# Kernel optimization log

Measured on AMD Instinct MI355X. Metric: run time of the kernel, lower is better.

## Reference

```python
import jax, jax.numpy as jnp
import numpy as np

EPS = 1e-5
SLOPE = 0.2  # leaky_relu negative_slope


def _mesh_conv_face(fe, gemm, w, b):
    # fe: [B, C, F]; gemm: [B, F, 3] neighbor face indices; w: [O, C, 4]; b: [O]
    # Gather 3 neighbor faces per face (irregular access).
    nb = jax.vmap(lambda f, g: f[:, g])(fe, gemm)  # [B, C, F, 3]
    n1, n2, n3 = nb[..., 0], nb[..., 1], nb[..., 2]
    # Symmetric (order-invariant) feature columns over the 3 neighbors.
    G = jnp.stack(
        [
            fe,                                                        # center face
            n1 + n2 + n3,                                              # sum
            jnp.abs(n1 - n2) + jnp.abs(n2 - n3) + jnp.abs(n3 - n1),    # pairwise abs-diff sum
            jnp.maximum(n1, jnp.maximum(n2, n3)),                      # max
        ],
        axis=-1,
    )  # [B, C, F, 4]
    # Conv2d with kernel (1,4) == contraction over (C, 4).
    return jnp.einsum('bcfk,ock->bof', G, w) + b[None, :, None]  # [B, O, F]


def _bn(x, gamma, beta):
    # BatchNorm2d (training mode) on [B, C, F]; normalize per-channel over (B, F).
    mu = x.mean(axis=(0, 2), keepdims=True)
    var = x.var(axis=(0, 2), keepdims=True)  # biased, as torch uses for normalization
    xn = (x - mu) * jax.lax.rsqrt(var + EPS)
    return gamma[None, :, None] * xn + beta[None, :, None]


def _lrelu(x):
    return jnp.where(x >= 0, x, SLOPE * x)


def setup_inputs() -> dict:
    key = jax.random.key(0)
    ks = jax.random.split(key, 8)
    B, Cin, Cout, F = 4, 32, 64, 50000
    fe = jax.random.normal(ks[0], (B, Cin, F), dtype=jnp.float32)
    gemm = jax.random.randint(ks[1], (B, F, 3), 0, F)
    w1 = jax.random.normal(ks[2], (Cout, Cin, 4), dtype=jnp.float32) * 0.05
    w2a = jax.random.normal(ks[3], (Cout, Cout, 4), dtype=jnp.float32) * 0.05
    w2b = jax.random.normal(ks[4], (Cout, Cout, 4), dtype=jnp.float32) * 0.05
    z = jnp.zeros((Cout,), jnp.float32)
    o = jnp.ones((Cout,), jnp.float32)
    return {
        'fe': fe, 'gemm': gemm,
        'w1': w1, 'b1': z, 'w2a': w2a, 'b2a': z, 'w2b': w2b, 'b2b': z,
        'g0': o, 'be0': z, 'g1': o, 'be1': z, 'g2': o, 'be2': z,
    }


def reference(fe, gemm, w1, b1, w2a, b2a, w2b, b2b, g0, be0, g1, be1, g2, be2):
    # conv1 -> BN -> LeakyReLU
    x1 = _lrelu(_bn(_mesh_conv_face(fe, gemm, w1, b1), g0, be0))
    # residual block 1
    x2 = _lrelu(_bn(_mesh_conv_face(x1, gemm, w2a, b2a), g1, be1) + x1)
    x1 = x2
    # residual block 2
    x2 = _lrelu(_bn(_mesh_conv_face(x1, gemm, w2b, b2b), g2, be2) + x1)
    return x2  # [B, Cout, F]; pool=0 so before_pool is None
```

## Files before the change

kernel.cpp:

```cpp
#include <hip/hip_runtime.h>
#include <hip/hip_bf16.h>
#include <math.h>


typedef __attribute__((ext_vector_type(8))) short short8;
typedef __attribute__((ext_vector_type(8))) unsigned short ushort8_t;
typedef __attribute__((ext_vector_type(4))) float f32x4;

__device__ inline unsigned short f2bf(float v) {
    union { float f; unsigned u; } x; x.f = v;
    unsigned r = x.u + 0x7fffu + ((x.u >> 16) & 1u);
    return (unsigned short)(r >> 16);
}
__device__ inline float bf2f(unsigned short u) {
    union { unsigned u; float f; } x; x.u = ((unsigned)u) << 16; return x.f;
}
__device__ inline unsigned pk2(float a, float b) {
    union { __hip_bfloat162 h; unsigned u; } c;
    c.h = __float22bfloat162_rn(make_float2(a, b));
    return c.u;
}

__global__ void transpose_fe_kernel(const float* __restrict__ fe,
                                    unsigned short* __restrict__ o, int F,
                                    const float* __restrict__ w1,
                                    const float* __restrict__ w2a,
                                    const float* __restrict__ w2b,
                                    unsigned short* __restrict__ w1b,
                                    unsigned short* __restrict__ w2ab,
                                    unsigned short* __restrict__ w2bb)
{
    __shared__ float tile[64 * 33];
    const int b = blockIdx.y;
    const int f0 = blockIdx.x * 64;
    const int t = threadIdx.x;

    {
        const int bid = blockIdx.y * gridDim.x + blockIdx.x;
        if (bid < 32)       { const int i = bid * 256 + t;        w1b[i]  = f2bf(w1[i]);  }
        else if (bid < 96)  { const int i = (bid - 32) * 256 + t; w2ab[i] = f2bf(w2a[i]); }
        else if (bid < 160) { const int i = (bid - 96) * 256 + t; w2bb[i] = f2bf(w2b[i]); }
    }

    const int lane = t & 63;
    const int w = t >> 6;
    const int f = f0 + lane;
    if (f < F) {
#pragma unroll
        for (int i = 0; i < 8; ++i) {
            const int c = w * 8 + i;
            tile[lane * 33 + c] = fe[((size_t)b * 32 + c) * F + f];
        }
    }
    __syncthreads();
    const int j = t >> 2, s = t & 3;
    const int fj = f0 + j;
    if (fj < F) {
        unsigned fw[4];
#pragma unroll
        for (int i = 0; i < 4; ++i)
            fw[i] = pk2(tile[j * 33 + s * 8 + 2 * i], tile[j * 33 + s * 8 + 2 * i + 1]);
        *(uint4*)(o + ((size_t)b * F + fj) * 32 + s * 8) = make_uint4(fw[0], fw[1], fw[2], fw[3]);
    }
}

template <int CIN, bool NORM>
__launch_bounds__(256, (CIN == 32) ? 5 : (NORM ? 3 : 4))
__global__ void conv_mfma_kernel(const unsigned short* __restrict__ x,
                                 const int*   __restrict__ gidx,
                                 const unsigned short* __restrict__ wb,
                                 const float* __restrict__ bias,
                                 const float* __restrict__ mrIn,
                                 unsigned short* __restrict__ y,
                                 float* __restrict__ pS,
                                 float* __restrict__ pQ,
                                 int nb, int nbx, int F)
{
    constexpr int NSEG = CIN / 32;
    constexpr int K    = 4 * CIN;
    constexpr int RB   = 2 * K;
    constexpr int GB   = 64 * RB;
    constexpr int GREG = (GB > 17408) ? GB : 17408;
    __shared__ __align__(16) unsigned char smem[GREG];
    float* tile = (float*)smem;

    const int NBg = gridDim.x;
    const int t = threadIdx.x;
    const int j = t >> 2, s = t & 3;
    const int lane = t & 63, wv = t >> 6;
    const int l15 = lane & 15, quad = lane >> 4;
    const int kb = quad * 8;

    unsigned char* grow = smem + j * RB;
    const int swz = (j & 7) << 4;

    const int bpx  = NBg >> 3;
    const int xcd  = blockIdx.x & 7, slot = blockIdx.x >> 3;
    const int qq   = nb >> 3, rr = nb & 7;
    const int lo   = (xcd < rr) ? xcd * (qq + 1) : rr * (qq + 1) + (xcd - rr) * qq;
    const int L    = qq + (xcd < rr ? 1 : 0);

    short8 afr[K / 32];
    {
        const int ar = wv * 16 + l15;
#pragma unroll
        for (int ksi = 0; ksi < K / 32; ++ksi)
            afr[ksi] = *(const short8*)(wb + (size_t)ar * K + ksi * 32 + kb);
    }
    const f32x4 bias4 = *(const f32x4*)(bias + wv * 16 + quad * 4);

    float scr[NSEG * 8], shr[NSEG * 8];
    if constexpr (NORM) {
#pragma unroll
        for (int i = 0; i < NSEG; ++i) {
            const int c0 = (i * 4 + s) * 8;
#pragma unroll
            for (int h = 0; h < 2; ++h) {
                const f32x4 a  = *(const f32x4*)(mrIn + c0 + 4 * h);
                const f32x4 sh = *(const f32x4*)(mrIn + 64 + c0 + 4 * h);
#pragma unroll
                for (int q = 0; q < 4; ++q) {
                    scr[i * 8 + 4 * h + q] = a[q];
                    shr[i * 8 + 4 * h + q] = sh[q];
                }
            }
        }
    }

    ushort8_t vc[NSEG], v0[NSEG], v1[NSEG], v2[NSEG];
    int gA0, gA1, gA2;
    float S_acc = 0.f, Q_acc = 0.f;
    const int so = t & 63, sg = t >> 6;

    int u = slot;

    if (u < L) {
        {
            const int tl = lo + u;
            const int b0 = tl / nbx;
            const int f0 = (tl - b0 * nbx) * 64;
            const int fc = min(f0 + j, F - 1);
            const int* gp = gidx + ((size_t)b0 * F + fc) * 3;
            const int g0 = gp[0], g1 = gp[1], g2 = gp[2];
            const unsigned short* xb = x + (size_t)b0 * F * CIN;
            const unsigned short* pc = xb + (size_t)fc * CIN;
            const unsigned short* p0 = xb + (size_t)g0 * CIN;
            const unsigned short* p1 = xb + (size_t)g1 * CIN;
            const unsigned short* p2 = xb + (size_t)g2 * CIN;
#pragma unroll
            for (int i = 0; i < NSEG; ++i) {
                const int c0 = (i * 4 + s) * 8;
                vc[i] = *(const ushort8_t*)(pc + c0);
                v0[i] = *(const ushort8_t*)(p0 + c0);
                v1[i] = *(const ushort8_t*)(p1 + c0);
                v2[i] = *(const ushort8_t*)(p2 + c0);
            }
        }
        {
            const int tn = lo + min(u + bpx, L - 1);
            const int bn = tn / nbx;
            const int fn = min((tn - bn * nbx) * 64 + j, F - 1);
            const int* gp = gidx + ((size_t)bn * F + fn) * 3;
            gA0 = gp[0]; gA1 = gp[1]; gA2 = gp[2];
        }
    }

    for (; u < L; u += bpx) {
        const int tl = lo + u;
        const int b  = tl / nbx;
        const int f0 = (tl - b * nbx) * 64;

#pragma unroll
        for (int i = 0; i < NSEG; ++i) {
            const int c0 = (i * 4 + s) * 8;
            unsigned fw[16];
#pragma unroll
            for (int q = 0; q < 8; ++q) {
                float ctr = bf2f(vc[i][q]);
                float a   = bf2f(v0[i][q]);
                float bb  = bf2f(v1[i][q]);
                float cc  = bf2f(v2[i][q]);
                if constexpr (NORM) {
                    const float sc_ = scr[i * 8 + q], sh_ = shr[i * 8 + q];
                    ctr = fmaf(ctr, sc_, sh_); ctr = fmaxf(ctr, 0.2f * ctr);
                    a   = fmaf(a,   sc_, sh_); a   = fmaxf(a,   0.2f * a);
                    bb  = fmaf(bb,  sc_, sh_); bb  = fmaxf(bb,  0.2f * bb);
                    cc  = fmaf(cc,  sc_, sh_); cc  = fmaxf(cc,  0.2f * cc);
                }
                const float su = a + bb + cc;
                const float dd = fabsf(a - bb) + fabsf(bb - cc) + fabsf(cc - a);
                const float mm = fmaxf(a, fmaxf(bb, cc));
                fw[2 * q]     = pk2(ctr, su);
                fw[2 * q + 1] = pk2(dd, mm);
            }
#pragma unroll
            for (int q4 = 0; q4 < 4; ++q4) {
                const int qb = 8 * c0 + 16 * q4;
                *(uint4*)(grow + (qb ^ swz)) =
                    make_uint4(fw[4 * q4], fw[4 * q4 + 1], fw[4 * q4 + 2], fw[4 * q4 + 3]);
            }
        }

        {
            const int tn = lo + min(u + bpx, L - 1);
            const int bn = tn / nbx;
            const int fcn = min((tn - bn * nbx) * 64 + j, F - 1);
            const unsigned short* xb = x + (size_t)bn * F * CIN;
            const unsigned short* pc = xb + (size_t)fcn * CIN;
            const unsigned short* p0 = xb + (size_t)gA0 * CIN;
            const unsigned short* p1 = xb + (size_t)gA1 * CIN;
            const unsigned short* p2 = xb + (size_t)gA2 * CIN;
#pragma unroll
            for (int i = 0; i < NSEG; ++i) {
                const int c0 = (i * 4 + s) * 8;
                vc[i] = *(const ushort8_t*)(pc + c0);
                v0[i] = *(const ushort8_t*)(p0 + c0);
                v1[i] = *(const ushort8_t*)(p1 + c0);
                v2[i] = *(const ushort8_t*)(p2 + c0);
            }
            const int t2 = lo + min(u + 2 * bpx, L - 1);
            const int b2 = t2 / nbx;
            const int f2 = min((t2 - b2 * nbx) * 64 + j, F - 1);
            const int* gp = gidx + ((size_t)b2 * F + f2) * 3;
            gA0 = gp[0]; gA1 = gp[1]; gA2 = gp[2];
        }
        __syncthreads();

        f32x4 acc[4];
#pragma unroll
        for (int nt = 0; nt < 4; ++nt) acc[nt] = (f32x4){0.f, 0.f, 0.f, 0.f};
#pragma unroll
        for (int ksi = 0; ksi < K / 32; ++ksi) {
            const int cb = 2 * (ksi * 32 + kb);
#pragma unroll
            for (int nt = 0; nt < 4; ++nt) {
                const int nr = nt * 16 + l15;
                const short8 bfr = *(const short8*)(smem + nr * RB + (cb ^ ((nr & 7) << 4)));
                acc[nt] = __builtin_amdgcn_mfma_f32_16x16x32_bf16(afr[ksi], bfr, acc[nt], 0, 0, 0);
            }
        }
        __syncthreads();

        {
            const int cb0 = wv * 16 + quad * 4;
#pragma unroll
            for (int nt = 0; nt < 4; ++nt) {
                const int face = nt * 16 + l15;
                *(f32x4*)(tile + face * 68 + cb0) = acc[nt] + bias4;
            }
        }
        __syncthreads();
        {
#pragma unroll
            for (int i = 0; i < 16; ++i) {
                const int f = sg + 4 * i;
                if (f0 + f < F) {
                    const float v = tile[f * 68 + so];
                    S_acc += v; Q_acc += v * v;
                }
            }
        }
        {
            const int f = f0 + j;
            if (f < F) {
                unsigned fw[8];
#pragma unroll
                for (int ii = 0; ii < 8; ++ii)
                    fw[ii] = pk2(tile[j * 68 + s * 16 + 2 * ii],
                                 tile[j * 68 + s * 16 + 2 * ii + 1]);
                unsigned short* yp = y + ((size_t)b * F + f) * 64 + s * 16;
                *(uint4*)yp       = make_uint4(fw[0], fw[1], fw[2], fw[3]);
                *(uint4*)(yp + 8) = make_uint4(fw[4], fw[5], fw[6], fw[7]);
            }
        }
        __syncthreads();
    }

    float* redS = (float*)smem;
    float* redQ = redS + 256;
    redS[t] = S_acc; redQ[t] = Q_acc;
    __syncthreads();
    if (t < 64) {
        pS[(size_t)blockIdx.x * 64 + t] = redS[t] + redS[64 + t] + redS[128 + t] + redS[192 + t];
        pQ[(size_t)blockIdx.x * 64 + t] = redQ[t] + redQ[64 + t] + redQ[128 + t] + redQ[192 + t];
    }
}

__global__ void finalize_kernel(const float* __restrict__ pS, const float* __restrict__ pQ,
                                int nbg, float invN,
                                const float* __restrict__ gamma,
                                const float* __restrict__ beta,
                                float* __restrict__ mr)
{
    __shared__ float rs_[256], rq_[256];
    const int o = blockIdx.x, t = threadIdx.x;
    float S = 0.f, Q = 0.f;
    for (int jj = t; jj < nbg; jj += 256) {
        S += pS[(size_t)jj * 64 + o];
        Q += pQ[(size_t)jj * 64 + o];
    }
    rs_[t] = S; rq_[t] = Q;
    __syncthreads();
#pragma unroll
    for (int s = 128; s > 0; s >>= 1) {
        if (t < s) { rs_[t] += rs_[t + s]; rq_[t] += rq_[t + s]; }
        __syncthreads();
    }
    if (t == 0) {
        const float mu  = rs_[0] * invN;
        const float var = rq_[0] * invN - mu * mu;
        const float rsg = rsqrtf(var + 1e-5f);
        const float sc  = gamma[o] * rsg;
        mr[o]      = sc;
        mr[64 + o] = fmaf(-sc, mu, beta[o]);
    }
}

__global__ void norm_res_kernel(const unsigned short* __restrict__ y1,
                                const unsigned short* __restrict__ y2,
                                const float* __restrict__ mr1,
                                const float* __restrict__ mr2,
                                unsigned short* __restrict__ out,
                                int N8)
{
    const int tid = blockIdx.x * blockDim.x + threadIdx.x;
    if (tid >= N8) return;
    const int c0 = (tid & 7) * 8;
    const ushort8_t a = *(const ushort8_t*)(y1 + (size_t)tid * 8);
    const ushort8_t b = *(const ushort8_t*)(y2 + (size_t)tid * 8);
    float r[8];
#pragma unroll
    for (int h = 0; h < 2; ++h) {
        const f32x4 s1 = *(const f32x4*)(mr1 + c0 + 4 * h);
        const f32x4 h1 = *(const f32x4*)(mr1 + 64 + c0 + 4 * h);
        const f32x4 s2 = *(const f32x4*)(mr2 + c0 + 4 * h);
        const f32x4 h2 = *(const f32x4*)(mr2 + 64 + c0 + 4 * h);
#pragma unroll
        for (int i = 0; i < 4; ++i) {
            float x1 = fmaf(bf2f(a[4 * h + i]), s1[i], h1[i]);
            x1 = fmaxf(x1, 0.2f * x1);
            float v = fmaf(bf2f(b[4 * h + i]), s2[i], h2[i]) + x1;
            r[4 * h + i] = fmaxf(v, 0.2f * v);
        }
    }
    unsigned fw[4];
#pragma unroll
    for (int i = 0; i < 4; ++i) fw[i] = pk2(r[2 * i], r[2 * i + 1]);
    *(uint4*)(out + (size_t)tid * 8) = make_uint4(fw[0], fw[1], fw[2], fw[3]);
}

__global__ void norm_transpose_kernel(const unsigned short* __restrict__ y,
                                      const unsigned short* __restrict__ res,
                                      const float* __restrict__ mr,
                                      float* __restrict__ out, int F)
{
    __shared__ float tile[64 * 65];
    const int b = blockIdx.y, f0 = blockIdx.x * 64, t = threadIdx.x;
    const int j = t >> 2, s = t & 3;
    const int f = f0 + j;
    if (f < F) {
        const size_t row = ((size_t)b * F + f) * 64;
#pragma unroll
        for (int i = 0; i < 2; ++i) {
            const int c0 = s * 16 + i * 8;
            const ushort8_t yv = *(const ushort8_t*)(y + row + c0);
            const ushort8_t rv = *(const ushort8_t*)(res + row + c0);
#pragma unroll
            for (int h = 0; h < 2; ++h) {
                const f32x4 sc = *(const f32x4*)(mr + c0 + 4 * h);
                const f32x4 sh = *(const f32x4*)(mr + 64 + c0 + 4 * h);
#pragma unroll
                for (int q = 0; q < 4; ++q) {
                    float vv = fmaf(bf2f(yv[4 * h + q]), sc[q], sh[q]) + bf2f(rv[4 * h + q]);
                    vv = fmaxf(vv, 0.2f * vv);
                    tile[(c0 + 4 * h + q) * 65 + j] = vv;
                }
            }
        }
    }
    __syncthreads();
    const int o = t >> 2;
    float* ob = out + ((size_t)b * 64 + o) * F + f0;
#pragma unroll
    for (int i = 0; i < 4; ++i) {
        const int fs = (i * 4 + s) * 4;
        if (f0 + fs < F) {
            f32x4 v;
#pragma unroll
            for (int q = 0; q < 4; ++q) v[q] = tile[o * 65 + fs + q];
            *(f32x4*)(ob + fs) = v;
        }
    }
}

extern "C" void kernel_launch(void* const* d_in, const int* in_sizes, int n_in,
                              void* d_out, int out_size, void* d_ws, size_t ws_size,
                              hipStream_t stream)
{
    const float* fe  = (const float*)d_in[0];
    const int*   gm  = (const int*)d_in[1];
    const float* w1  = (const float*)d_in[2];
    const float* b1  = (const float*)d_in[3];
    const float* w2a = (const float*)d_in[4];
    const float* b2a = (const float*)d_in[5];
    const float* w2b = (const float*)d_in[6];
    const float* b2b = (const float*)d_in[7];
    const float* g0  = (const float*)d_in[8];
    const float* be0 = (const float*)d_in[9];
    const float* g1  = (const float*)d_in[10];
    const float* be1 = (const float*)d_in[11];
    const float* g2  = (const float*)d_in[12];
    const float* be2 = (const float*)d_in[13];

    const int B = 4, O = 64;
    const int F = in_sizes[0] / (B * 32);
    const int M = B * F;
    const float invN = 1.0f / (float)M;
    const int nbx = (F + 63) / 64;
    const int nb  = nbx * B;

    unsigned short* Y1 = (unsigned short*)d_ws;
    unsigned short* Y2 = Y1 + (size_t)M * O;
    unsigned short* x2 = Y2 + (size_t)M * O;
    float* pS  = (float*)(x2 + (size_t)M * O);
    float* pQ  = pS + 2048 * 64;
    float* mr1 = pQ + 2048 * 64;
    float* mr2 = mr1 + 128;
    float* mr3 = mr2 + 128;
    unsigned short* w1b  = (unsigned short*)(mr3 + 128);
    unsigned short* w2ab = w1b + 64 * 128;
    unsigned short* w2bb = w2ab + 64 * 256;
    unsigned short* fe_t = (unsigned short*)d_out;

    dim3 blk(256);
    dim3 tgrid(nbx, B);
    const int N8 = M * 8;
    dim3 ngrid((N8 + 255) / 256);
    const int g1g = (nb < 1280) ? (nb & ~7) : 1280;
    const int g2g = (nb < 768)  ? (nb & ~7) : 768;
    const int g3g = (nb < 1024) ? (nb & ~7) : 1024;

    transpose_fe_kernel<<<tgrid, blk, 0, stream>>>(fe, fe_t, F,
                                                   w1, w2a, w2b, w1b, w2ab, w2bb);

    conv_mfma_kernel<32, false><<<g1g, blk, 0, stream>>>(
        fe_t, gm, w1b, b1, nullptr, Y1, pS, pQ, nb, nbx, F);
    finalize_kernel<<<64, 256, 0, stream>>>(pS, pQ, g1g, invN, g0, be0, mr1);

    conv_mfma_kernel<64, true><<<g2g, blk, 0, stream>>>(
        Y1, gm, w2ab, b2a, mr1, Y2, pS, pQ, nb, nbx, F);
    finalize_kernel<<<64, 256, 0, stream>>>(pS, pQ, g2g, invN, g1, be1, mr2);

    norm_res_kernel<<<ngrid, blk, 0, stream>>>(Y1, Y2, mr1, mr2, x2, N8);

    conv_mfma_kernel<64, false><<<g3g, blk, 0, stream>>>(
        x2, gm, w2bb, b2b, nullptr, Y1, pS, pQ, nb, nbx, F);
    finalize_kernel<<<64, 256, 0, stream>>>(pS, pQ, g3g, invN, g2, be2, mr3);

    norm_transpose_kernel<<<tgrid, blk, 0, stream>>>(Y1, x2, mr3, (float*)d_out, F);
}
```

Measured before the change: 216.3 us.

## Double-buffer neighbor gathers with ping-pong register sets in conv loop

Replaces the single register set for gathered center/neighbor features with two alternating sets (A/B). The gather for the next tile is issued before the current tile's feature build and MFMA, not after it. The loop is manually unrolled by two via macros. The aim is to hide more irregular gather latency behind compute. The cost is doubled gather registers, which may lower occupancy or cause spills, especially for CIN=64.

Result: slower. 232.8 us (+7.6%).

```diff
diff --git a/kernel.cpp b/kernel.cpp
--- a/kernel.cpp
+++ b/kernel.cpp
@@ -63,6 +63,119 @@
         *(uint4*)(o + ((size_t)b * F + fj) * 32 + s * 8) = make_uint4(fw[0], fw[1], fw[2], fw[3]);
     }
 }
+
+#define LOAD_IDX(gg0, gg1, gg2, TT) do {                                   \
+    const int tn_ = lo + min((TT), L - 1);                                 \
+    const int bn_ = tn_ / nbx;                                             \
+    const int fn_ = min((tn_ - bn_ * nbx) * 64 + j, F - 1);                \
+    const int* gp_ = gidx + ((size_t)bn_ * F + fn_) * 3;                   \
+    gg0 = gp_[0]; gg1 = gp_[1]; gg2 = gp_[2];                              \
+} while (0)
+
+#define ISSUE_G(SET, gg0, gg1, gg2, TT) do {                               \
+    const int tn_ = lo + min((TT), L - 1);                                 \
+    const int bn_ = tn_ / nbx;                                             \
+    const int fcn_ = min((tn_ - bn_ * nbx) * 64 + j, F - 1);               \
+    const unsigned short* xb_ = x + (size_t)bn_ * F * CIN;                 \
+    const unsigned short* pc_ = xb_ + (size_t)fcn_ * CIN;                  \
+    const unsigned short* p0_ = xb_ + (size_t)(gg0) * CIN;                 \
+    const unsigned short* p1_ = xb_ + (size_t)(gg1) * CIN;                 \
+    const unsigned short* p2_ = xb_ + (size_t)(gg2) * CIN;                 \
+    _Pragma("unroll")                                                      \
+    for (int i_ = 0; i_ < NSEG; ++i_) {                                    \
+        const int c0_ = (i_ * 4 + s) * 8;                                  \
+        SET##c[i_]  = *(const ushort8_t*)(pc_ + c0_);                      \
+        SET##n0[i_] = *(const ushort8_t*)(p0_ + c0_);                      \
+        SET##n1[i_] = *(const ushort8_t*)(p1_ + c0_);                      \
+        SET##n2[i_] = *(const ushort8_t*)(p2_ + c0_);                      \
+    }                                                                      \
+} while (0)
+
+#define TILE_BODY(SET, go0, go1, go2, gn0, gn1, gn2, UU) do {              \
+    const int tl_ = lo + (UU);                                             \
+    const int b_  = tl_ / nbx;                                             \
+    const int f0_ = (tl_ - b_ * nbx) * 64;                                 \
+    LOAD_IDX(gn0, gn1, gn2, (UU) + 2 * bpx);                               \
+    _Pragma("unroll")                                                      \
+    for (int i_ = 0; i_ < NSEG; ++i_) {                                    \
+        const int c0_ = (i_ * 4 + s) * 8;                                  \
+        unsigned fw_[16];                                                  \
+        _Pragma("unroll")                                                  \
+        for (int q_ = 0; q_ < 8; ++q_) {                                   \
+            float ctr_ = bf2f(SET##c[i_][q_]);                             \
+            float a_   = bf2f(SET##n0[i_][q_]);                            \
+            float bb_  = bf2f(SET##n1[i_][q_]);                            \
+            float cc_  = bf2f(SET##n2[i_][q_]);                            \
+            if constexpr (NORM) {                                          \
+                const float sc_ = scr[i_ * 8 + q_], sh_ = shr[i_ * 8 + q_];\
+                ctr_ = fmaf(ctr_, sc_, sh_); ctr_ = fmaxf(ctr_, 0.2f * ctr_);\
+                a_   = fmaf(a_,   sc_, sh_); a_   = fmaxf(a_,   0.2f * a_);\
+                bb_  = fmaf(bb_,  sc_, sh_); bb_  = fmaxf(bb_,  0.2f * bb_);\
+                cc_  = fmaf(cc_,  sc_, sh_); cc_  = fmaxf(cc_,  0.2f * cc_);\
+            }                                                              \
+            const float su_ = a_ + bb_ + cc_;                              \
+            const float dd_ = fabsf(a_ - bb_) + fabsf(bb_ - cc_) + fabsf(cc_ - a_);\
+            const float mm_ = fmaxf(a_, fmaxf(bb_, cc_));                  \
+            fw_[2 * q_]     = pk2(ctr_, su_);                              \
+            fw_[2 * q_ + 1] = pk2(dd_, mm_);                               \
+        }                                                                  \
+        _Pragma("unroll")                                                  \
+        for (int q4_ = 0; q4_ < 4; ++q4_) {                                \
+            const int qb_ = 8 * c0_ + 16 * q4_;                            \
+            *(uint4*)(grow + (qb_ ^ swz)) =                                \
+                make_uint4(fw_[4 * q4_], fw_[4 * q4_ + 1],                 \
+                           fw_[4 * q4_ + 2], fw_[4 * q4_ + 3]);            \
+        }                                                                  \
+    }                                                                      \
+    __syncthreads();                                      \
+    f32x4 acc_[4];                                                         \
+    _Pragma("unroll")                                                      \
+    for (int nt_ = 0; nt_ < 4; ++nt_) acc_[nt_] = (f32x4){0.f,0.f,0.f,0.f};\
+    _Pragma("unroll")                                                      \
+    for (int ksi_ = 0; ksi_ < K / 32; ++ksi_) {                            \
+        const int cb_ = 2 * (ksi_ * 32 + kb);                              \
+        _Pragma("unroll")                                                  \
+        for (int nt_ = 0; nt_ < 4; ++nt_) {                                \
+            const int nr_ = nt_ * 16 + l15;                                \
+            const short8 bfr_ = *(const short8*)(smem + nr_ * RB + (cb_ ^ ((nr_ & 7) << 4)));\
+            acc_[nt_] = __builtin_amdgcn_mfma_f32_16x16x32_bf16(afr[ksi_], bfr_, acc_[nt_], 0, 0, 0);\
+        }                                                                  \
+    }                                                                      \
+    __syncthreads();                                    \
+    {                                                                      \
+        const int cb0_ = wv * 16 + quad * 4;                               \
+        _Pragma("unroll")                                                  \
+        for (int nt_ = 0; nt_ < 4; ++nt_) {                                \
+            const int face_ = nt_ * 16 + l15;                              \
+            *(f32x4*)(tile + face_ * 68 + cb0_) = acc_[nt_] + bias4;       \
+        }                                                                  \
+    }                                                                      \
+    __syncthreads();                                   \
+    {                                                                      \
+        _Pragma("unroll")                                                  \
+        for (int i_ = 0; i_ < 16; ++i_) {                                  \
+            const int f_ = sg + 4 * i_;                                    \
+            if (f0_ + f_ < F) {                                            \
+                const float v_ = tile[f_ * 68 + so];                       \
+                S_acc += v_; Q_acc += v_ * v_;                             \
+            }                                                              \
+        }                                                                  \
+    }                                                                      \
+    {                                                                      \
+        const int f_ = f0_ + j;                                            \
+        if (f_ < F) {                                                      \
+            unsigned fw_[8];                                               \
+            _Pragma("unroll")                                              \
+            for (int ii_ = 0; ii_ < 8; ++ii_)                              \
+                fw_[ii_] = pk2(tile[j * 68 + s * 16 + 2 * ii_],            \
+                               tile[j * 68 + s * 16 + 2 * ii_ + 1]);       \
+            unsigned short* yp_ = y + ((size_t)b_ * F + f_) * 64 + s * 16; \
+            *(uint4*)yp_       = make_uint4(fw_[0], fw_[1], fw_[2], fw_[3]);\
+            *(uint4*)(yp_ + 8) = make_uint4(fw_[4], fw_[5], fw_[6], fw_[7]);\
+        }                                                                  \
+    }                                                                      \
+    __syncthreads();                                    \
+} while (0)
 
 template <int CIN, bool NORM>
 __launch_bounds__(256, (CIN == 32) ? 5 : (NORM ? 3 : 4))
@@ -127,155 +240,30 @@
         }
     }
 
-    ushort8_t vc[NSEG], v0[NSEG], v1[NSEG], v2[NSEG];
-    int gA0, gA1, gA2;
+    ushort8_t Ac[NSEG], An0[NSEG], An1[NSEG], An2[NSEG];
+    ushort8_t Bc[NSEG], Bn0[NSEG], Bn1[NSEG], Bn2[NSEG];
+    int gA0, gA1, gA2, gB0, gB1, gB2;
     float S_acc = 0.f, Q_acc = 0.f;
     const int so = t & 63, sg = t >> 6;
 
     int u = slot;
-
     if (u < L) {
-        {
-            const int tl = lo + u;
-            const int b0 = tl / nbx;
-            const int f0 = (tl - b0 * nbx) * 64;
-            const int fc = min(f0 + j, F - 1);
-            const int* gp = gidx + ((size_t)b0 * F + fc) * 3;
-            const int g0 = gp[0], g1 = gp[1], g2 = gp[2];
-            const unsigned short* xb = x + (size_t)b0 * F * CIN;
-            const unsigned short* pc = xb + (size_t)fc * CIN;
-            const unsigned short* p0 = xb + (size_t)g0 * CIN;
-            const unsigned short* p1 = xb + (size_t)g1 * CIN;
-            const unsigned short* p2 = xb + (size_t)g2 * CIN;
-#pragma unroll
-            for (int i = 0; i < NSEG; ++i) {
-                const int c0 = (i * 4 + s) * 8;
-                vc[i] = *(const ushort8_t*)(pc + c0);
-                v0[i] = *(const ushort8_t*)(p0 + c0);
-                v1[i] = *(const ushort8_t*)(p1 + c0);
-                v2[i] = *(const ushort8_t*)(p2 + c0);
-            }
-        }
-        {
-            const int tn = lo + min(u + bpx, L - 1);
-            const int bn = tn / nbx;
-            const int fn = min((tn - bn * nbx) * 64 + j, F - 1);
-            const int* gp = gidx + ((size_t)bn * F + fn) * 3;
-            gA0 = gp[0]; gA1 = gp[1]; gA2 = gp[2];
-        }
-    }
-
-    for (; u < L; u += bpx) {
-        const int tl = lo + u;
-        const int b  = tl / nbx;
-        const int f0 = (tl - b * nbx) * 64;
-
-#pragma unroll
-        for (int i = 0; i < NSEG; ++i) {
-            const int c0 = (i * 4 + s) * 8;
-            unsigned fw[16];
-#pragma unroll
-            for (int q = 0; q < 8; ++q) {
-                float ctr = bf2f(vc[i][q]);
-                float a   = bf2f(v0[i][q]);
-                float bb  = bf2f(v1[i][q]);
-                float cc  = bf2f(v2[i][q]);
-                if constexpr (NORM) {
-                    const float sc_ = scr[i * 8 + q], sh_ = shr[i * 8 + q];
-                    ctr = fmaf(ctr, sc_, sh_); ctr = fmaxf(ctr, 0.2f * ctr);
-                    a   = fmaf(a,   sc_, sh_); a   = fmaxf(a,   0.2f * a);
-                    bb  = fmaf(bb,  sc_, sh_); bb  = fmaxf(bb,  0.2f * bb);
-                    cc  = fmaf(cc,  sc_, sh_); cc  = fmaxf(cc,  0.2f * cc);
-                }
-                const float su = a + bb + cc;
-                const float dd = fabsf(a - bb) + fabsf(bb - cc) + fabsf(cc - a);
-                const float mm = fmaxf(a, fmaxf(bb, cc));
-                fw[2 * q]     = pk2(ctr, su);
-                fw[2 * q + 1] = pk2(dd, mm);
-            }
-#pragma unroll
-            for (int q4 = 0; q4 < 4; ++q4) {
-                const int qb = 8 * c0 + 16 * q4;
-                *(uint4*)(grow + (qb ^ swz)) =
-                    make_uint4(fw[4 * q4], fw[4 * q4 + 1], fw[4 * q4 + 2], fw[4 * q4 + 3]);
-            }
-        }
-
-        {
-            const int tn = lo + min(u + bpx, L - 1);
-            const int bn = tn / nbx;
-            const int fcn = min((tn - bn * nbx) * 64 + j, F - 1);
-            const unsigned short* xb = x + (size_t)bn * F * CIN;
-            const unsigned short* pc = xb + (size_t)fcn * CIN;
-            const unsigned short* p0 = xb + (size_t)gA0 * CIN;
-            const unsigned short* p1 = xb + (size_t)gA1 * CIN;
-            const unsigned short* p2 = xb + (size_t)gA2 * CIN;
-#pragma unroll
-            for (int i = 0; i < NSEG; ++i) {
-                const int c0 = (i * 4 + s) * 8;
-                vc[i] = *(const ushort8_t*)(pc + c0);
-                v0[i] = *(const ushort8_t*)(p0 + c0);
-                v1[i] = *(const ushort8_t*)(p1 + c0);
-                v2[i] = *(const ushort8_t*)(p2 + c0);
-            }
-            const int t2 = lo + min(u + 2 * bpx, L - 1);
-            const int b2 = t2 / nbx;
-            const int f2 = min((t2 - b2 * nbx) * 64 + j, F - 1);
-            const int* gp = gidx + ((size_t)b2 * F + f2) * 3;
-            gA0 = gp[0]; gA1 = gp[1]; gA2 = gp[2];
-        }
-        __syncthreads();
-
-        f32x4 acc[4];
-#pragma unroll
-        for (int nt = 0; nt < 4; ++nt) acc[nt] = (f32x4){0.f, 0.f, 0.f, 0.f};
-#pragma unroll
-        for (int ksi = 0; ksi < K / 32; ++ksi) {
-            const int cb = 2 * (ksi * 32 + kb);
-#pragma unroll
-            for (int nt = 0; nt < 4; ++nt) {
-                const int nr = nt * 16 + l15;
-                const short8 bfr = *(const short8*)(smem + nr * RB + (cb ^ ((nr & 7) << 4)));
-                acc[nt] = __builtin_amdgcn_mfma_f32_16x16x32_bf16(afr[ksi], bfr, acc[nt], 0, 0, 0);
-            }
-        }
-        __syncthreads();
-
-        {
-            const int cb0 = wv * 16 + quad * 4;
-#pragma unroll
-            for (int nt = 0; nt < 4; ++nt) {
-                const int face = nt * 16 + l15;
-                *(f32x4*)(tile + face * 68 + cb0) = acc[nt] + bias4;
-            }
-        }
-        __syncthreads();
-        {
-#pragma unroll
-            for (int i = 0; i < 16; ++i) {
-                const int f = sg + 4 * i;
-                if (f0 + f < F) {
-                    const float v = tile[f * 68 + so];
-                    S_acc += v; Q_acc += v * v;
-                }
-            }
-        }
-        {
-            const int f = f0 + j;
-            if (f < F) {
-                unsigned fw[8];
-#pragma unroll
-                for (int ii = 0; ii < 8; ++ii)
-                    fw[ii] = pk2(tile[j * 68 + s * 16 + 2 * ii],
-                                 tile[j * 68 + s * 16 + 2 * ii + 1]);
-                unsigned short* yp = y + ((size_t)b * F + f) * 64 + s * 16;
-                *(uint4*)yp       = make_uint4(fw[0], fw[1], fw[2], fw[3]);
-                *(uint4*)(yp + 8) = make_uint4(fw[4], fw[5], fw[6], fw[7]);
-            }
-        }
-        __syncthreads();
-    }
-
+        LOAD_IDX(gA0, gA1, gA2, u);
+        ISSUE_G(A, gA0, gA1, gA2, u);
+        LOAD_IDX(gB0, gB1, gB2, u + bpx);
+        while (true) {
+            ISSUE_G(B, gB0, gB1, gB2, u + bpx);
+            TILE_BODY(A, gB0, gB1, gB2, gA0, gA1, gA2, u);
+            u += bpx;
+            if (u >= L) break;
+            ISSUE_G(A, gA0, gA1, gA2, u + bpx);
+            TILE_BODY(B, gA0, gA1, gA2, gB0, gB1, gB2, u);
+            u += bpx;
+            if (u >= L) break;
+        }
+    }
+
+    __syncthreads();
     float* redS = (float*)smem;
     float* redQ = redS + 256;
     redS[t] = S_acc; redQ[t] = Q_acc;
```
